# Optimization experiments

Hardware: AMD Instinct MI355X
Metric: run time of the kernel (lower is better)

## Reference

```python
import jax, jax.numpy as jnp
import numpy as np

N = 100000   # nodes (word + doc)
E = 1600000  # edges
IN = 256     # in_feats
H = 64       # n_hidden
MH = 64      # mlp_hidden
C = 16       # n_classes


def setup_inputs() -> dict:
    key = jax.random.key(0)
    ks = jax.random.split(key, 12)
    s = lambda f: 1.0 / np.sqrt(f)
    return {
        "x": jax.random.normal(ks[0], (N, IN), jnp.float32),
        "edge_index": jax.random.randint(ks[1], (2, E), 0, N, dtype=jnp.int64),
        "edge_weight": jax.random.uniform(ks[2], (E,), jnp.float32),
        "W1": jax.random.normal(ks[3], (IN, H), jnp.float32) * s(IN),
        "b1": jnp.zeros((H,), jnp.float32),
        "W2": jax.random.normal(ks[4], (H, H), jnp.float32) * s(H),
        "b2": jnp.zeros((H,), jnp.float32),
        "Wm1": jax.random.normal(ks[5], (H, MH), jnp.float32) * s(H),
        "bm1": jnp.zeros((MH,), jnp.float32),
        "Wm2": jax.random.normal(ks[6], (MH, C), jnp.float32) * s(MH),
        "bm2": jnp.zeros((C,), jnp.float32),
    }


def _gcn_norm(edge_index, edge_weight, n):
    # PyG GCNConv: add self-loops (weight 1), symmetric normalization
    loops = jnp.arange(n, dtype=edge_index.dtype)
    src = jnp.concatenate([edge_index[0], loops])
    dst = jnp.concatenate([edge_index[1], loops])
    w = jnp.concatenate([edge_weight, jnp.ones((n,), edge_weight.dtype)])
    deg = jax.ops.segment_sum(w, dst, num_segments=n)
    dinv = jnp.where(deg > 0, jax.lax.rsqrt(deg), 0.0)
    norm = dinv[src] * w * dinv[dst]
    return src, dst, norm


def _gcn_conv(x, W, b, src, dst, norm, n):
    h = x @ W                           # [N, out]
    msg = h[src] * norm[:, None]        # gather + scale, [E+N, out]
    agg = jax.ops.segment_sum(msg, dst, num_segments=n)
    return agg + b


def reference(x, edge_index, edge_weight, W1, b1, W2, b2, Wm1, bm1, Wm2, bm2):
    src, dst, norm = _gcn_norm(edge_index, edge_weight, N)
    # GCN stack (eval mode: dropout is identity)
    h = jax.nn.relu(_gcn_conv(x, W1, b1, src, dst, norm, N))
    h = jax.nn.relu(_gcn_conv(h, W2, b2, src, dst, norm, N))
    # MLP head
    h = jax.nn.relu(h @ Wm1 + bm1)
    logits = h @ Wm2 + bm2
    return jax.nn.softmax(logits, axis=-1)
```

## Files before the change

### kernel.cpp

```cpp
#include <hip/hip_runtime.h>
#include <cstdint>
#include <cstddef>

#define NN 100000
#define NE 1600000
#define IN_F 256
#define HD 64
#define NC 16

#define NT 391
#define NBLK 196
#define EPB 8192
#define CM (NT * NBLK)
#define SCB 75



__global__ __launch_bounds__(256) void k_count(const int* __restrict__ dstA,
                                               int* __restrict__ counts) {
    __shared__ int hist[NT];
    int tid = threadIdx.x;
    for (int t = tid; t < NT; t += 256) hist[t] = 0;
    __syncthreads();
    int base = blockIdx.x * EPB;
#pragma unroll
    for (int i = 0; i < 32; ++i) {
        int e = base + i * 256 + tid;
        if (e < NE) atomicAdd(&hist[dstA[e] >> 8], 1);
    }
    __syncthreads();
    for (int t = tid; t < NT; t += 256)
        counts[t * NBLK + blockIdx.x] = hist[t];
}

__global__ __launch_bounds__(256) void k_scan1(int* __restrict__ c,
                                               int* __restrict__ bsum) {
    __shared__ int ss[256];
    int t = threadIdx.x;
    int base = blockIdx.x * 1024 + t * 4;
    int c0 = (base + 0 < CM) ? c[base + 0] : 0;
    int c1 = (base + 1 < CM) ? c[base + 1] : 0;
    int c2 = (base + 2 < CM) ? c[base + 2] : 0;
    int c3 = (base + 3 < CM) ? c[base + 3] : 0;
    int tsum = c0 + c1 + c2 + c3;
    ss[t] = tsum;
    __syncthreads();
    for (int off = 1; off < 256; off <<= 1) {
        int v = (t >= off) ? ss[t - off] : 0;
        __syncthreads();
        ss[t] += v;
        __syncthreads();
    }
    int excl = ss[t] - tsum;
    if (t == 255) bsum[blockIdx.x] = ss[255];
    if (base + 0 < CM) c[base + 0] = excl;
    if (base + 1 < CM) c[base + 1] = excl + c0;
    if (base + 2 < CM) c[base + 2] = excl + c0 + c1;
    if (base + 3 < CM) c[base + 3] = excl + c0 + c1 + c2;
}

__global__ __launch_bounds__(128) void k_scan2(const int* __restrict__ bsum,
                                               int* __restrict__ bpref) {
    __shared__ int ss[128];
    int t = threadIdx.x;
    int v = (t < SCB) ? bsum[t] : 0;
    ss[t] = v;
    __syncthreads();
    for (int off = 1; off < 128; off <<= 1) {
        int u = (t >= off) ? ss[t - off] : 0;
        __syncthreads();
        ss[t] += u;
        __syncthreads();
    }
    if (t < SCB) bpref[t] = ss[t] - v;
}

__global__ __launch_bounds__(256) void k_scan3(int* __restrict__ c,
                                               const int* __restrict__ bpref) {
    int i = blockIdx.x * 256 + threadIdx.x;
    if (i < CM) c[i] += bpref[i >> 10];
}

template <bool FULL>
__global__ __launch_bounds__(256) void k_fill2(const int* __restrict__ srcA,
                                               const int* __restrict__ dstA,
                                               const float* __restrict__ ew,
                                               const int* __restrict__ counts,
                                               int2* __restrict__ tmp) {
    __shared__ int basel[NT];
    int tid = threadIdx.x;
    for (int t = tid; t < NT; t += 256) basel[t] = counts[t * NBLK + blockIdx.x];
    __syncthreads();
    int eb = blockIdx.x * EPB;
#pragma unroll
    for (int i = 0; i < 32; ++i) {
        int e = eb + i * 256 + tid;
        if (e < NE) {
            int d = dstA[e];
            int pos = atomicAdd(&basel[d >> 8], 1);
            if (FULL)
                tmp[pos] = make_int2(srcA[e] | ((d & 255) << 17),
                                     __float_as_int(ew[e]));
            else
                tmp[pos] = make_int2(e, d & 255);
        }
    }
}

template <bool FULL>
__global__ __launch_bounds__(256) void k_sort(const int* __restrict__ counts,
                                              const int2* __restrict__ tmp,
                                              int2* __restrict__ outP,
                                              int* __restrict__ outE,
                                              int* __restrict__ rowptr,
                                              const float* __restrict__ ew,
                                              float* __restrict__ dinv) {
    __shared__ int hist[256], ss[256], bases[256];
    int tid = threadIdx.x;
    int tile = blockIdx.x;
    int bs = counts[tile * NBLK];
    int be = (tile + 1 < NT) ? counts[(tile + 1) * NBLK] : NE;
    hist[tid] = 0;
    __syncthreads();
    for (int p = bs + tid; p < be; p += 256) {
        int dl = FULL ? ((tmp[p].x >> 17) & 255) : tmp[p].y;
        atomicAdd(&hist[dl], 1);
    }
    __syncthreads();
    int v = hist[tid];
    ss[tid] = v;
    __syncthreads();
    for (int off = 1; off < 256; off <<= 1) {
        int u = (tid >= off) ? ss[tid - off] : 0;
        __syncthreads();
        ss[tid] += u;
        __syncthreads();
    }
    int excl = ss[tid] - v;
    bases[tid] = bs + excl;
    int row = tile * 256 + tid;
    if (row < NN) rowptr[row] = bs + excl;
    if (tile == NT - 1 && tid == 0) rowptr[NN] = NE;
    __syncthreads();
    for (int p = bs + tid; p < be; p += 256) {
        int2 t2 = tmp[p];
        int dl = FULL ? ((t2.x >> 17) & 255) : t2.y;
        int pos = atomicAdd(&bases[dl], 1);
        if (FULL) outP[pos] = t2;
        else      outE[pos] = t2.x;
    }
    __syncthreads();
    if (row < NN) {
        int p0 = bs + excl, p1 = bs + excl + v;
        float s = 1.0f;
        for (int p = p0; p < p1; ++p)
            s += FULL ? __int_as_float(outP[p].y) : ew[outE[p]];
        dinv[row] = rsqrtf(s);
    }
}

template <bool FULL>
__global__ __launch_bounds__(256) void k_agg(const int* __restrict__ rowptr,
                                             const int2* __restrict__ pairsS,
                                             const int* __restrict__ eid,
                                             const int* __restrict__ srcA,
                                             const float* __restrict__ ew,
                                             const float* __restrict__ dinv,
                                             const float* __restrict__ g,
                                             float* __restrict__ agg) {
    int row = blockIdx.x * 4 + (threadIdx.x >> 6);
    int lane = threadIdx.x & 63;
    if (row >= NN) return;
    int p = rowptr[row], pe = rowptr[row + 1];
    float di = dinv[row];
    float acc = g[(size_t)row * HD + lane];
    if (FULL) {
        for (; p + 4 <= pe; p += 4) {
            int2 v0 = pairsS[p], v1 = pairsS[p + 1],
                 v2 = pairsS[p + 2], v3 = pairsS[p + 3];
            int s0 = v0.x & 0x1FFFF, s1 = v1.x & 0x1FFFF,
                s2 = v2.x & 0x1FFFF, s3 = v3.x & 0x1FFFF;
            float g0 = g[(size_t)s0 * HD + lane];
            float g1 = g[(size_t)s1 * HD + lane];
            float g2 = g[(size_t)s2 * HD + lane];
            float g3 = g[(size_t)s3 * HD + lane];
            acc = fmaf(__int_as_float(v0.y), g0, acc);
            acc = fmaf(__int_as_float(v1.y), g1, acc);
            acc = fmaf(__int_as_float(v2.y), g2, acc);
            acc = fmaf(__int_as_float(v3.y), g3, acc);
        }
        for (; p < pe; ++p) {
            int2 v = pairsS[p];
            int s = v.x & 0x1FFFF;
            acc = fmaf(__int_as_float(v.y), g[(size_t)s * HD + lane], acc);
        }
    } else {
        for (; p + 4 <= pe; p += 4) {
            int e0 = eid[p], e1 = eid[p + 1], e2 = eid[p + 2], e3 = eid[p + 3];
            int s0 = srcA[e0], s1 = srcA[e1], s2 = srcA[e2], s3 = srcA[e3];
            float g0 = g[(size_t)s0 * HD + lane];
            float g1 = g[(size_t)s1 * HD + lane];
            float g2 = g[(size_t)s2 * HD + lane];
            float g3 = g[(size_t)s3 * HD + lane];
            acc = fmaf(ew[e0], g0, acc);
            acc = fmaf(ew[e1], g1, acc);
            acc = fmaf(ew[e2], g2, acc);
            acc = fmaf(ew[e3], g3, acc);
        }
        for (; p < pe; ++p) {
            int e = eid[p];
            acc = fmaf(ew[e], g[(size_t)srcA[e] * HD + lane], acc);
        }
    }
    agg[(size_t)row * HD + lane] = di * acc;
}

template <bool SCALE>
__global__ __launch_bounds__(256, 6) void k_gemm1(const float* __restrict__ x,
                                                  const float* __restrict__ W1,
                                                  const float* __restrict__ dinv,
                                                  float* __restrict__ h0) {
    __shared__ float sW[64 * HD];
    int tid = threadIdx.x;
    int rs  = tid >> 4;
    int cg  = tid & 15;
    int base = blockIdx.x * 64;
    int rowc[4];
    bool rv[4];
#pragma unroll
    for (int r = 0; r < 4; ++r) {
        int row = base + rs + 16 * r;
        rv[r] = row < NN;
        rowc[r] = rv[r] ? row : (NN - 1);
    }
    float acc[4][4];
#pragma unroll
    for (int r = 0; r < 4; ++r)
#pragma unroll
        for (int c = 0; c < 4; ++c) acc[r][c] = 0.0f;

    for (int kc = 0; kc < IN_F; kc += 64) {
        __syncthreads();
        {
            const float4* wsrc = (const float4*)(W1 + (size_t)kc * HD);
            float4* wdst = (float4*)sW;
#pragma unroll
            for (int q = 0; q < 4; ++q) wdst[q * 256 + tid] = wsrc[q * 256 + tid];
        }
        __syncthreads();
        for (int k4 = 0; k4 < 16; ++k4) {
            float xs[4][4];
#pragma unroll
            for (int r = 0; r < 4; ++r)
                *(float4*)xs[r] = *(const float4*)(x + (size_t)rowc[r] * IN_F + kc + k4 * 4);
#pragma unroll
            for (int j = 0; j < 4; ++j) {
                float wv[4];
                *(float4*)wv = *(const float4*)(sW + (k4 * 4 + j) * HD + cg * 4);
#pragma unroll
                for (int r = 0; r < 4; ++r) {
                    float xj = xs[r][j];
#pragma unroll
                    for (int c = 0; c < 4; ++c) acc[r][c] = fmaf(xj, wv[c], acc[r][c]);
                }
            }
        }
    }
#pragma unroll
    for (int r = 0; r < 4; ++r) {
        if (!rv[r]) continue;
        float di = SCALE ? dinv[rowc[r]] : 1.0f;
        *(float4*)(h0 + (size_t)rowc[r] * HD + cg * 4) =
            make_float4(acc[r][0] * di, acc[r][1] * di,
                        acc[r][2] * di, acc[r][3] * di);
    }
}

template <bool BIASRELU, bool SCALEOUT>
__global__ __launch_bounds__(256, 6) void k_gemm64(const float* __restrict__ in,
                                                   const float* __restrict__ bin,
                                                   const float* __restrict__ W,
                                                   const float* __restrict__ bout,
                                                   const float* __restrict__ dinv,
                                                   float* __restrict__ outA) {
    __shared__ float sW[HD * HD];
    __shared__ float sBin[HD];
    int tid = threadIdx.x;
    int rs  = tid >> 4;
    int cg  = tid & 15;
    int base = blockIdx.x * 64;
    int rowc[4];
    bool rv[4];
#pragma unroll
    for (int r = 0; r < 4; ++r) {
        int row = base + rs + 16 * r;
        rv[r] = row < NN;
        rowc[r] = rv[r] ? row : (NN - 1);
    }
    {
        const float4* wsrc = (const float4*)W;
        float4* wdst = (float4*)sW;
#pragma unroll
        for (int q = 0; q < 4; ++q) wdst[q * 256 + tid] = wsrc[q * 256 + tid];
        if (tid < 16) ((float4*)sBin)[tid] = ((const float4*)bin)[tid];
    }
    __syncthreads();
    float acc[4][4];
#pragma unroll
    for (int r = 0; r < 4; ++r)
#pragma unroll
        for (int c = 0; c < 4; ++c) acc[r][c] = 0.0f;

    for (int k4 = 0; k4 < 16; ++k4) {
        float bs[4];
        *(float4*)bs = ((const float4*)sBin)[k4];
        float xs[4][4];
#pragma unroll
        for (int r = 0; r < 4; ++r)
            *(float4*)xs[r] = *(const float4*)(in + (size_t)rowc[r] * HD + k4 * 4);
#pragma unroll
        for (int j = 0; j < 4; ++j) {
            float wv[4];
            *(float4*)wv = *(const float4*)(sW + (k4 * 4 + j) * HD + cg * 4);
#pragma unroll
            for (int r = 0; r < 4; ++r) {
                float hv = fmaxf(xs[r][j] + bs[j], 0.0f);
#pragma unroll
                for (int c = 0; c < 4; ++c) acc[r][c] = fmaf(hv, wv[c], acc[r][c]);
            }
        }
    }
#pragma unroll
    for (int r = 0; r < 4; ++r) {
        if (!rv[r]) continue;
        float* ha = outA + (size_t)rowc[r] * HD + cg * 4;
        if (BIASRELU) {
            float bo[4];
            *(float4*)bo = *(const float4*)(bout + cg * 4);
            *(float4*)ha = make_float4(fmaxf(acc[r][0] + bo[0], 0.0f),
                                       fmaxf(acc[r][1] + bo[1], 0.0f),
                                       fmaxf(acc[r][2] + bo[2], 0.0f),
                                       fmaxf(acc[r][3] + bo[3], 0.0f));
        } else {
            float di = SCALEOUT ? dinv[rowc[r]] : 1.0f;
            *(float4*)ha = make_float4(acc[r][0] * di, acc[r][1] * di,
                                       acc[r][2] * di, acc[r][3] * di);
        }
    }
}

__global__ __launch_bounds__(256) void k_init_fb(float* __restrict__ deg) {
    int i = blockIdx.x * 256 + threadIdx.x;
    if (i < NN) deg[i] = 1.0f;
}
__global__ __launch_bounds__(256) void k_edge_fb(const int* __restrict__ dst,
                                                 const float* __restrict__ ew,
                                                 float* __restrict__ deg) {
    int e = blockIdx.x * 256 + threadIdx.x;
    if (e < NE) atomicAdd(&deg[dst[e]], ew[e]);
}
__global__ __launch_bounds__(256) void k_dinv_fb(float* __restrict__ deg) {
    int i = blockIdx.x * 256 + threadIdx.x;
    if (i < NN) {
        float d = deg[i];
        deg[i] = d > 0.0f ? rsqrtf(d) : 0.0f;
    }
}
__global__ __launch_bounds__(256) void k_selfloop(const float* __restrict__ h,
                                                  const float* __restrict__ dinv,
                                                  float* __restrict__ agg) {
    int i = blockIdx.x * 256 + threadIdx.x;
    if (i >= NN * (HD / 4)) return;
    int row = i / (HD / 4);
    float di = dinv[row];
    float d2 = di * di;
    float4 v = ((const float4*)h)[i];
    ((float4*)agg)[i] = make_float4(v.x * d2, v.y * d2, v.z * d2, v.w * d2);
}
__global__ __launch_bounds__(256) void k_scatter(const int* __restrict__ src,
                                                 const int* __restrict__ dst,
                                                 const float* __restrict__ ew,
                                                 const float* __restrict__ dinv,
                                                 const float* __restrict__ h,
                                                 float* __restrict__ agg) {
    int e = blockIdx.x * 4 + (threadIdx.x >> 6);
    int lane = threadIdx.x & 63;
    if (e >= NE) return;
    int s = src[e];
    int d = dst[e];
    float nrm = dinv[s] * ew[e] * dinv[d];
    float v = h[(size_t)s * HD + lane] * nrm;
    atomicAdd(&agg[(size_t)d * HD + lane], v);
}

__global__ __launch_bounds__(256, 4) void k_out(const float* __restrict__ h3,
                                                const float* __restrict__ Wm2,
                                                const float* __restrict__ bm2,
                                                float* __restrict__ out) {
    __shared__ float sW[HD * NC];
    int tid = threadIdx.x;
    ((float4*)sW)[tid] = ((const float4*)Wm2)[tid];
    __syncthreads();
    int row = blockIdx.x * 256 + tid;
    bool rv = row < NN;
    int rowc = rv ? row : (NN - 1);
    float acc[16];
#pragma unroll
    for (int c = 0; c < 16; ++c) acc[c] = 0.0f;

    for (int k4 = 0; k4 < 16; ++k4) {
        float xs[4];
        *(float4*)xs = *(const float4*)(h3 + (size_t)rowc * HD + k4 * 4);
#pragma unroll
        for (int j = 0; j < 4; ++j) {
            float wv[16];
            const float4* wr4 = (const float4*)(sW + (k4 * 4 + j) * NC);
#pragma unroll
            for (int q = 0; q < 4; ++q) ((float4*)wv)[q] = wr4[q];
            float xj = xs[j];
#pragma unroll
            for (int c = 0; c < 16; ++c) acc[c] = fmaf(xj, wv[c], acc[c]);
        }
    }
    if (!rv) return;
    float bm[16];
#pragma unroll
    for (int q = 0; q < 4; ++q) ((float4*)bm)[q] = ((const float4*)bm2)[q];
    float l[16];
#pragma unroll
    for (int c = 0; c < 16; ++c) l[c] = acc[c] + bm[c];
    float m = l[0];
#pragma unroll
    for (int c = 1; c < 16; ++c) m = fmaxf(m, l[c]);
    float ssum = 0.0f;
#pragma unroll
    for (int c = 0; c < 16; ++c) {
        l[c] = expf(l[c] - m);
        ssum += l[c];
    }
    float inv = 1.0f / ssum;
    float4* op = (float4*)(out + (size_t)rowc * NC);
#pragma unroll
    for (int q = 0; q < 4; ++q)
        op[q] = make_float4(l[q * 4] * inv, l[q * 4 + 1] * inv,
                            l[q * 4 + 2] * inv, l[q * 4 + 3] * inv);
}

extern "C" void kernel_launch(void* const* d_in, const int* in_sizes, int n_in,
                              void* d_out, int out_size, void* d_ws, size_t ws_size,
                              hipStream_t stream) {
    const float* x   = (const float*)d_in[0];
    const int*   ei  = (const int*)d_in[1];
    const float* ew  = (const float*)d_in[2];
    const float* W1  = (const float*)d_in[3];
    const float* b1  = (const float*)d_in[4];
    const float* W2  = (const float*)d_in[5];
    const float* b2  = (const float*)d_in[6];
    const float* Wm1 = (const float*)d_in[7];
    const float* bm1 = (const float*)d_in[8];
    const float* Wm2 = (const float*)d_in[9];
    const float* bm2 = (const float*)d_in[10];
    float* out = (float*)d_out;

    char* base = (char*)d_ws;
    float* dinv   = (float*)base;
    float* A      = (float*)(base + 400128);
    float* B      = (float*)(base + 26000128);
    int*   rowptr = (int*)(base + 51600128);
    int2*  pairsS = (int2*)(base + 52000256);
    int2*  tmp    = (int2*)(base + 400128);
    int*   counts = (int*)(base + 26000128);
    int*   bsum   = (int*)(base + 26000128 + 306544);
    int*   bpref  = (int*)(base + 26000128 + 306944);

    const int* src = ei;
    const int* dst = ei + NE;

    const bool full  = ws_size >= (size_t)64800912;
    const bool douta = !full && ws_size >= (size_t)52000912;
    const int g_node = (NN + 255) / 256;
    const int g_g1   = (NN + 63) / 64;
    const int g_g64  = (NN + 63) / 64;
    const int g_agg  = (NN + 3) / 4;
    const int g_red  = (NN * (HD / 4) + 255) / 256;
    const int g_out  = (NN + 255) / 256;
    int* eid = (int*)d_out;

    if (full || douta) {
        k_count<<<dim3(NBLK), dim3(256), 0, stream>>>(dst, counts);
        k_scan1<<<dim3(SCB), dim3(256), 0, stream>>>(counts, bsum);
        k_scan2<<<dim3(1), dim3(128), 0, stream>>>(bsum, bpref);
        k_scan3<<<dim3((CM + 255) / 256), dim3(256), 0, stream>>>(counts, bpref);
        if (full) {
            k_fill2<true><<<dim3(NBLK), dim3(256), 0, stream>>>(src, dst, ew, counts, tmp);
            k_sort<true><<<dim3(NT), dim3(256), 0, stream>>>(counts, tmp, pairsS, nullptr, rowptr, ew, dinv);
        } else {
            k_fill2<false><<<dim3(NBLK), dim3(256), 0, stream>>>(src, dst, ew, counts, tmp);
            k_sort<false><<<dim3(NT), dim3(256), 0, stream>>>(counts, tmp, nullptr, eid, rowptr, ew, dinv);
        }
        k_gemm1<true><<<dim3(g_g1), dim3(256), 0, stream>>>(x, W1, dinv, A);
        if (full)
            k_agg<true><<<dim3(g_agg), dim3(256), 0, stream>>>(rowptr, pairsS, nullptr, src, ew, dinv, A, B);
        else
            k_agg<false><<<dim3(g_agg), dim3(256), 0, stream>>>(rowptr, nullptr, eid, src, ew, dinv, A, B);
        k_gemm64<false, true><<<dim3(g_g64), dim3(256), 0, stream>>>(B, b1, W2, nullptr, dinv, A);
        if (full)
            k_agg<true><<<dim3(g_agg), dim3(256), 0, stream>>>(rowptr, pairsS, nullptr, src, ew, dinv, A, B);
        else
            k_agg<false><<<dim3(g_agg), dim3(256), 0, stream>>>(rowptr, nullptr, eid, src, ew, dinv, A, B);
        k_gemm64<true, false><<<dim3(g_g64), dim3(256), 0, stream>>>(B, b2, Wm1, bm1, dinv, A);
        k_out<<<dim3(g_out), dim3(256), 0, stream>>>(A, Wm2, bm2, out);
    } else {
        k_init_fb<<<dim3(g_node), dim3(256), 0, stream>>>(dinv);
        k_edge_fb<<<dim3(NE / 256), dim3(256), 0, stream>>>(dst, ew, dinv);
        k_dinv_fb<<<dim3(g_node), dim3(256), 0, stream>>>(dinv);
        k_gemm1<false><<<dim3(g_g1), dim3(256), 0, stream>>>(x, W1, dinv, A);
        k_selfloop<<<dim3(g_red), dim3(256), 0, stream>>>(A, dinv, B);
        k_scatter<<<dim3(NE / 4), dim3(256), 0, stream>>>(src, dst, ew, dinv, A, B);
        k_gemm64<false, false><<<dim3(g_g64), dim3(256), 0, stream>>>(B, b1, W2, nullptr, dinv, A);
        k_selfloop<<<dim3(g_red), dim3(256), 0, stream>>>(A, dinv, B);
        k_scatter<<<dim3(NE / 4), dim3(256), 0, stream>>>(src, dst, ew, dinv, A, B);
        k_gemm64<true, false><<<dim3(g_g64), dim3(256), 0, stream>>>(B, b2, Wm1, bm1, dinv, A);
        k_out<<<dim3(g_out), dim3(256), 0, stream>>>(A, Wm2, bm2, out);
    }
}
```

Measured before the change: 515.2 us.

## Retile first GEMM to 128-row blocks with shared-memory staged X

The first-layer GEMM (x @ W1) now processes 128 rows per block with a 4x8 register tile per thread. A 32-wide K slice of x is staged into shared memory in transposed form, alongside the matching W1 slice. Previously each thread read x directly from global memory as strided float4 loads. The intent is more FMA work per load and coalesced x reads, at the cost of higher register and LDS use, lower occupancy (launch bounds 6 to 4), and possible LDS bank conflicts on the transposed stores.

```diff
diff --git a/kernel.cpp b/kernel.cpp
--- a/kernel.cpp
+++ b/kernel.cpp
@@ -216,63 +216,70 @@
 }
 
 template <bool SCALE>
-__global__ __launch_bounds__(256, 6) void k_gemm1(const float* __restrict__ x,
+__global__ __launch_bounds__(256, 4) void k_gemm1(const float* __restrict__ x,
                                                   const float* __restrict__ W1,
                                                   const float* __restrict__ dinv,
                                                   float* __restrict__ h0) {
-    __shared__ float sW[64 * HD];
+    __shared__ float sX[32 * 128];
+    __shared__ float sW[32 * 64];
     int tid = threadIdx.x;
-    int rs  = tid >> 4;
-    int cg  = tid & 15;
-    int base = blockIdx.x * 64;
-    int rowc[4];
-    bool rv[4];
-#pragma unroll
-    for (int r = 0; r < 4; ++r) {
-        int row = base + rs + 16 * r;
-        rv[r] = row < NN;
-        rowc[r] = rv[r] ? row : (NN - 1);
-    }
-    float acc[4][4];
+    int rs  = tid >> 3;
+    int cg  = tid & 7;
+    int base = blockIdx.x * 128;
+
+    int f4   = tid >> 5;
+    int srow = tid & 31;
+
+    float acc[4][8];
 #pragma unroll
     for (int r = 0; r < 4; ++r)
 #pragma unroll
-        for (int c = 0; c < 4; ++c) acc[r][c] = 0.0f;
-
-    for (int kc = 0; kc < IN_F; kc += 64) {
+        for (int c = 0; c < 8; ++c) acc[r][c] = 0.0f;
+
+    for (int kc = 0; kc < IN_F; kc += 32) {
         __syncthreads();
         {
             const float4* wsrc = (const float4*)(W1 + (size_t)kc * HD);
             float4* wdst = (float4*)sW;
 #pragma unroll
-            for (int q = 0; q < 4; ++q) wdst[q * 256 + tid] = wsrc[q * 256 + tid];
-        }
-        __syncthreads();
-        for (int k4 = 0; k4 < 16; ++k4) {
-            float xs[4][4];
-#pragma unroll
-            for (int r = 0; r < 4; ++r)
-                *(float4*)xs[r] = *(const float4*)(x + (size_t)rowc[r] * IN_F + kc + k4 * 4);
-#pragma unroll
-            for (int j = 0; j < 4; ++j) {
-                float wv[4];
-                *(float4*)wv = *(const float4*)(sW + (k4 * 4 + j) * HD + cg * 4);
-#pragma unroll
-                for (int r = 0; r < 4; ++r) {
-                    float xj = xs[r][j];
-#pragma unroll
-                    for (int c = 0; c < 4; ++c) acc[r][c] = fmaf(xj, wv[c], acc[r][c]);
-                }
+            for (int q = 0; q < 2; ++q) wdst[q * 256 + tid] = wsrc[q * 256 + tid];
+        }
+#pragma unroll
+        for (int q = 0; q < 4; ++q) {
+            int grow = q * 32 + srow;
+            int growc = (base + grow < NN) ? (base + grow) : (NN - 1);
+            float4 v = *(const float4*)(x + (size_t)growc * IN_F + kc + f4 * 4);
+            sX[(f4 * 4 + 0) * 128 + grow] = v.x;
+            sX[(f4 * 4 + 1) * 128 + grow] = v.y;
+            sX[(f4 * 4 + 2) * 128 + grow] = v.z;
+            sX[(f4 * 4 + 3) * 128 + grow] = v.w;
+        }
+        __syncthreads();
+#pragma unroll 4
+        for (int k = 0; k < 32; ++k) {
+            float xs[4];
+            *(float4*)xs = *(const float4*)(sX + k * 128 + rs * 4);
+            float wv[8];
+            *(float4*)(wv + 0) = *(const float4*)(sW + k * HD + cg * 8);
+            *(float4*)(wv + 4) = *(const float4*)(sW + k * HD + cg * 8 + 4);
+#pragma unroll
+            for (int r = 0; r < 4; ++r) {
+                float xj = xs[r];
+#pragma unroll
+                for (int c = 0; c < 8; ++c) acc[r][c] = fmaf(xj, wv[c], acc[r][c]);
             }
         }
     }
 #pragma unroll
     for (int r = 0; r < 4; ++r) {
-        if (!rv[r]) continue;
-        float di = SCALE ? dinv[rowc[r]] : 1.0f;
-        *(float4*)(h0 + (size_t)rowc[r] * HD + cg * 4) =
-            make_float4(acc[r][0] * di, acc[r][1] * di,
-                        acc[r][2] * di, acc[r][3] * di);
+        int row = base + rs * 4 + r;
+        if (row >= NN) continue;
+        float di = SCALE ? dinv[row] : 1.0f;
+        float* hp = h0 + (size_t)row * HD + cg * 8;
+        *(float4*)(hp + 0) = make_float4(acc[r][0] * di, acc[r][1] * di,
+                                         acc[r][2] * di, acc[r][3] * di);
+        *(float4*)(hp + 4) = make_float4(acc[r][4] * di, acc[r][5] * di,
+                                         acc[r][6] * di, acc[r][7] * di);
     }
 }
 
@@ -479,7 +486,7 @@
     const bool full  = ws_size >= (size_t)64800912;
     const bool douta = !full && ws_size >= (size_t)52000912;
     const int g_node = (NN + 255) / 256;
-    const int g_g1   = (NN + 63) / 64;
+    const int g_g1   = (NN + 127) / 128;
     const int g_g64  = (NN + 63) / 64;
     const int g_agg  = (NN + 3) / 4;
     const int g_red  = (NN * (HD / 4) + 255) / 256;
```

Measured after the change: 490.4 us. -4.8%, faster.
